# Kernel tuning notes

Measured on AMD Instinct MI355X. Metric: run time of the kernel, lower is better.

## Reference

```python
import jax, jax.numpy as jnp
import numpy as np

DIM = 1024        # model dim
HEADS = 1         # num_heads (fc1 in_features==1 forces this)
HDIM = DIM // HEADS
INNER = 16        # dim_inner
B, L = 2, 4096
ROPE_BASE = 32.0


def _apply_rope(x, pos, base):
    # x: [b, l, h, d]; standard rotate-half RoPE
    d = x.shape[-1]
    inv_freq = base ** (-jnp.arange(0, d, 2, dtype=jnp.float32) / d)   # [d/2]
    ang = pos[:, None].astype(jnp.float32) * inv_freq                  # [l, d/2]
    emb = jnp.concatenate([ang, ang], axis=-1)                         # [l, d]
    cos = jnp.cos(emb)[None, :, None, :].astype(x.dtype)
    sin = jnp.sin(emb)[None, :, None, :].astype(x.dtype)
    x1, x2 = x[..., : d // 2], x[..., d // 2:]
    rot = jnp.concatenate([-x2, x1], axis=-1)
    return x * cos + rot * sin


def setup_inputs() -> dict:
    key = jax.random.key(0)
    ks = jax.random.split(key, 7)
    hidden_states = jax.random.normal(ks[0], (B, L, DIM), dtype=jnp.float32)
    Wq = jax.random.normal(ks[1], (DIM, DIM), dtype=jnp.float32) * 0.02
    Wk = jax.random.normal(ks[2], (DIM, DIM), dtype=jnp.float32) * 0.02
    fc1_w = jax.random.normal(ks[3], (INNER, 1), dtype=jnp.float32) * 0.1
    fc1_b = jax.random.normal(ks[4], (INNER,), dtype=jnp.float32) * 0.1
    fc2_w = jax.random.normal(ks[5], (DIM, INNER), dtype=jnp.float32) * 0.1
    fc2_b = jax.random.normal(ks[6], (DIM,), dtype=jnp.float32) * 0.1
    return {"hidden_states": hidden_states, "Wq": Wq, "Wk": Wk,
            "fc1_w": fc1_w, "fc1_b": fc1_b, "fc2_w": fc2_w, "fc2_b": fc2_b}


def reference(hidden_states, Wq, Wk, fc1_w, fc1_b, fc2_w, fc2_b):
    b, l, _ = hidden_states.shape
    # projections, cast to bf16 as in the torch module
    q = (hidden_states @ Wq.T).reshape(b, l, HEADS, HDIM).astype(jnp.bfloat16)
    k = (hidden_states @ Wk.T).reshape(b, l, HEADS, HDIM).astype(jnp.bfloat16)
    pos = jnp.arange(l)
    q = _apply_rope(q, pos, ROPE_BASE)
    k = _apply_rope(k, pos, ROPE_BASE)
    # causal exp(QK) with NO softmax normalization; accumulate in fp32
    scores = jnp.einsum('bqhd,bkhd->bhqk',
                        q.astype(jnp.float32), k.astype(jnp.float32)) / (HDIM ** 0.5)
    causal = jnp.tril(jnp.ones((l, l), dtype=bool))                    # [l, l]
    exp_qk = jnp.where(causal[None, None], jnp.exp(scores), 0.0)       # [b, h, l, l]
    o = jnp.swapaxes(exp_qk.sum(axis=-1), 1, 2)                        # [b, l, h]
    # small MLP: h(=1) -> INNER -> DIM
    o = jax.nn.relu(o @ fc1_w.T + fc1_b)
    return o @ fc2_w.T + fc2_b                                         # [b, l, DIM]
```

## Files before the change

kernel.cpp:

```cpp
#include <hip/hip_runtime.h>
#include <hip/hip_bf16.h>

typedef __bf16 bf16_t;
typedef __bf16 bf16x4 __attribute__((ext_vector_type(4)));
typedef __bf16 bf16x8 __attribute__((ext_vector_type(8)));
typedef float f32x4 __attribute__((ext_vector_type(4)));

#define B_   2
#define L_   4096
#define DIM_ 1024
#define M_   (B_ * L_)
#define NTASK2_ 272

__device__ __forceinline__ void ld_g2l_16(const bf16_t* g, bf16_t* l) {
  __builtin_amdgcn_global_load_lds(
      (__attribute__((address_space(1))) void*)g,
      (__attribute__((address_space(3))) void*)l, 16, 0, 0);
}

__global__ void cvt_all(const float* __restrict__ hs, const float* __restrict__ wq,
                        const float* __restrict__ wk, bf16_t* __restrict__ hs_b,
                        bf16_t* __restrict__ wq_b, bf16_t* __restrict__ wk_b,
                        float* __restrict__ o) {
  const int N_HS = M_ * DIM_ / 4, N_W = DIM_ * DIM_ / 4;
  int i = blockIdx.x * blockDim.x + threadIdx.x;
  if (i < M_ / 4) ((float4*)o)[i] = float4{0.f, 0.f, 0.f, 0.f};
  const float* s; bf16_t* d; int idx;
  if (i < N_HS)            { s = hs; d = hs_b; idx = i; }
  else if (i < N_HS + N_W) { s = wq; d = wq_b; idx = i - N_HS; }
  else                     { s = wk; d = wk_b; idx = i - N_HS - N_W; }
  float4 v = ((const float4*)s)[idx];
  bf16x4 ov = { (bf16_t)v.x, (bf16_t)v.y, (bf16_t)v.z, (bf16_t)v.w };
  ((bf16x4*)d)[idx] = ov;
}

template <int BSEGS>
__device__ __forceinline__ void core256(const bf16_t* __restrict__ A,
                                        const bf16_t* __restrict__ B0,
                                        const bf16_t* __restrict__ B1,
                                        bf16_t* sm, bool active,
                                        f32x4 (&acc)[4][BSEGS / 2]) {
  constexpr int SEGS = 16 + BSEGS;
  constexpr int BUF  = SEGS * 512;
  const int tid  = threadIdx.x;
  const int wave = tid >> 6, lane = tid & 63;
  const int wm = wave >> 1, wn = wave & 1;
  const int quad = lane >> 4, l16 = lane & 15;
  const int srow = lane >> 2;
  const int scol = (((lane & 3) ^ ((lane >> 3) & 3)) * 8);
  const int rsw  = ((l16 >> 1) & 3) * 8;
  const int loff = l16 * 32 + ((quad * 8) ^ rsw);

  const bf16_t* gA0 = A + (size_t)(wave * 16 + srow) * DIM_ + scol;
  const bf16_t* gA1 = A + (size_t)((wave + 8) * 16 + srow) * DIM_ + scol;
  const bf16_t* gB0 = B0 + (size_t)(wave * 16 + srow) * DIM_ + scol;
  const bf16_t* gB1 = gB0;
  if constexpr (BSEGS == 16) gB1 = B1 + (size_t)(wave * 16 + srow) * DIM_ + scol;

  bf16_t* p0 = sm;
  bf16_t* p1 = sm + BUF;
  bf16_t* p2 = sm + 2 * BUF;

  auto stage = [&](int kk, bf16_t* buf) {
    ld_g2l_16(gA0 + kk, buf + wave * 512);
    ld_g2l_16(gA1 + kk, buf + (wave + 8) * 512);
    ld_g2l_16(gB0 + kk, buf + (16 + wave) * 512);
    if constexpr (BSEGS == 16) ld_g2l_16(gB1 + kk, buf + (24 + wave) * 512);
  };

  stage(0, p0);
  stage(32, p1);
  if constexpr (BSEGS == 16) asm volatile("s_waitcnt vmcnt(4)" ::: "memory");
  else                       asm volatile("s_waitcnt vmcnt(3)" ::: "memory");
  __builtin_amdgcn_s_barrier();

  for (int s = 0; s < 32; ++s) {
    bf16x8 aF[4], bF[BSEGS / 2];
    if (active) {
#pragma unroll
      for (int rf = 0; rf < 4; ++rf)
        aF[rf] = *(const bf16x8*)(p0 + (wm * 4 + rf) * 512 + loff);
#pragma unroll
      for (int cf = 0; cf < BSEGS / 2; ++cf) {
        int k = (cf & 3) + wn * 4 + (cf >> 2) * 8;
        bF[cf] = *(const bf16x8*)(p0 + (16 + k) * 512 + loff);
      }
    }
    if (s < 30) stage((s + 2) * 32, p2);
    __builtin_amdgcn_s_barrier();
    asm volatile("s_waitcnt lgkmcnt(0)" ::: "memory");
    __builtin_amdgcn_sched_barrier(0);
    if (active) {
      __builtin_amdgcn_s_setprio(1);
#pragma unroll
      for (int rf = 0; rf < 4; ++rf)
#pragma unroll
        for (int cf = 0; cf < BSEGS / 2; ++cf)
          acc[rf][cf] = __builtin_amdgcn_mfma_f32_16x16x32_bf16(
              aF[rf], bF[cf], acc[rf][cf], 0, 0, 0);
      __builtin_amdgcn_s_setprio(0);
    }
    if (s < 30) {
      if constexpr (BSEGS == 16) asm volatile("s_waitcnt vmcnt(4)" ::: "memory");
      else                       asm volatile("s_waitcnt vmcnt(3)" ::: "memory");
    } else if (s == 30) {
      asm volatile("s_waitcnt vmcnt(0)" ::: "memory");
    }
    __builtin_amdgcn_s_barrier();
    bf16_t* t0 = p0; p0 = p1; p1 = p2; p2 = t0;
  }
}

__global__ __launch_bounds__(512, 2)
void proj_gemm(const bf16_t* __restrict__ A, const bf16_t* __restrict__ Wqb,
               const bf16_t* __restrict__ Wkb, bf16_t* __restrict__ Cq,
               bf16_t* __restrict__ Ck) {
  __shared__ __attribute__((aligned(16))) bf16_t sm[3 * 32 * 512];
  const int bid = blockIdx.x;
  const int xcd = bid & 7, slot = bid >> 3;
  const int m0 = (xcd * 4 + (slot >> 3)) * 256;
  const int zn = slot & 7;
  const int z = zn >> 2, n0 = (zn & 3) * 128;
  const bf16_t* Wb = z ? Wkb : Wqb;
  bf16_t* Cm = z ? Ck : Cq;

  f32x4 acc[4][8] = {};
  core256<16>(A + (size_t)m0 * DIM_, Wb + (size_t)n0 * DIM_,
              Wb + (size_t)(n0 + 512) * DIM_, sm, true, acc);

  const int tid = threadIdx.x, wave = tid >> 6, lane = tid & 63;
  const int wm = wave >> 1, wn = wave & 1;
  const int quad = lane >> 4, l16 = lane & 15;

  float inv[4];
#pragma unroll
  for (int cf = 0; cf < 4; ++cf) {
    int j = n0 + wn * 64 + cf * 16 + l16;
    inv[cf] = exp2f((float)j * (-5.0f / 512.0f));
  }
#pragma unroll
  for (int rf = 0; rf < 4; ++rf)
#pragma unroll
    for (int r = 0; r < 4; ++r) {
      int m = m0 + wm * 64 + rf * 16 + quad * 4 + r;
      float posf = (float)(m & (L_ - 1));
#pragma unroll
      for (int cf = 0; cf < 4; ++cf) {
        int j = n0 + wn * 64 + cf * 16 + l16;
        float ang = posf * inv[cf];
        float c = cosf(ang), s = sinf(ang);
        float cb = (float)(bf16_t)c, sb = (float)(bf16_t)s;
        float x1 = (float)(bf16_t)acc[rf][cf][r];
        float x2 = (float)(bf16_t)acc[rf][cf + 4][r];
        Cm[(size_t)m * DIM_ + j]       = (bf16_t)(x1 * cb - x2 * sb);
        Cm[(size_t)m * DIM_ + j + 512] = (bf16_t)(x2 * cb + x1 * sb);
      }
    }
}

__global__ __launch_bounds__(512, 4)
void attn_rowsum(const bf16_t* __restrict__ Q, const bf16_t* __restrict__ Kc,
                 float* __restrict__ o) {
  __shared__ __attribute__((aligned(16))) bf16_t sm[3 * 24 * 512];
  int logical = (blockIdx.x & 7) * 68 + (blockIdx.x >> 3);
  int b = logical / NTASK2_;
  int t = logical - b * NTASK2_;
  int mi = (int)((sqrtf(4.0f * (float)t + 1.0f) - 1.0f) * 0.5f);
  while ((mi + 1) * (mi + 2) <= t) ++mi;
  while (mi * (mi + 1) > t) --mi;
  int nt = t - mi * (mi + 1);

  const int tid = threadIdx.x, wave = tid >> 6, lane = tid & 63;
  const int wm = wave >> 1, wn = wave & 1;
  const int quad = lane >> 4, l16 = lane & 15;

  const bf16_t* A  = Q  + (size_t)b * L_ * DIM_ + (size_t)mi * 256 * DIM_;
  const bf16_t* Bp = Kc + (size_t)b * L_ * DIM_ + (size_t)nt * 128 * DIM_;

  bool active = (mi * 256 + wm * 64 + 63) >= nt * 128;

  f32x4 acc[4][4] = {};
  core256<8>(A, Bp, nullptr, sm, active, acc);

  if (active) {
    const bool masked = (nt >= 2 * mi);
#pragma unroll
    for (int rf = 0; rf < 4; ++rf) {
#pragma unroll
      for (int r = 0; r < 4; ++r) {
        int grow = mi * 256 + wm * 64 + rf * 16 + quad * 4 + r;
        float sum = 0.0f;
#pragma unroll
        for (int cf = 0; cf < 4; ++cf) {
          int gcol = nt * 128 + wn * 64 + cf * 16 + l16;
          float e = __expf(acc[rf][cf][r] * 0.03125f);
          if (!masked || gcol <= grow) sum += e;
        }
        sum += __shfl_xor(sum, 1);
        sum += __shfl_xor(sum, 2);
        sum += __shfl_xor(sum, 4);
        sum += __shfl_xor(sum, 8);
        if (l16 == 0)
          atomicAdd(&o[b * L_ + grow], sum);
      }
    }
  }
}

__global__ __launch_bounds__(256)
void mlp_out_kernel(const float* __restrict__ o, const float* __restrict__ fc1_w,
                    const float* __restrict__ fc1_b, const float* __restrict__ fc2_w,
                    const float* __restrict__ fc2_b, float* __restrict__ out) {
  const int R = 16;
  int row0 = blockIdx.x * R;
  int tid = threadIdx.x;
  __shared__ float h[R][16];
  {
    int rl = tid >> 4, i = tid & 15;
    float s = o[row0 + rl];
    h[rl][i] = fmaxf(fc1_w[i] * s + fc1_b[i], 0.0f);
  }
  __syncthreads();
  int d = tid * 4;
  float w[4][16];
#pragma unroll
  for (int c = 0; c < 4; ++c)
#pragma unroll
    for (int i = 0; i < 16; ++i) w[c][i] = fc2_w[(d + c) * 16 + i];
  float4 bb = *(const float4*)(fc2_b + d);
  for (int rl = 0; rl < R; ++rl) {
    float4 v = bb;
#pragma unroll
    for (int i = 0; i < 16; ++i) {
      float hv = h[rl][i];
      v.x += w[0][i] * hv; v.y += w[1][i] * hv;
      v.z += w[2][i] * hv; v.w += w[3][i] * hv;
    }
    *(float4*)(out + (size_t)(row0 + rl) * DIM_ + d) = v;
  }
}

extern "C" void kernel_launch(void* const* d_in, const int* in_sizes, int n_in,
                              void* d_out, int out_size, void* d_ws, size_t ws_size,
                              hipStream_t stream) {
  const float* hs    = (const float*)d_in[0];
  const float* Wq    = (const float*)d_in[1];
  const float* Wk    = (const float*)d_in[2];
  const float* fc1_w = (const float*)d_in[3];
  const float* fc1_b = (const float*)d_in[4];
  const float* fc2_w = (const float*)d_in[5];
  const float* fc2_b = (const float*)d_in[6];
  float* out = (float*)d_out;

  char* ws = (char*)d_ws;
  bf16_t* hs_bf = (bf16_t*)ws; ws += (size_t)M_ * DIM_ * 2;
  bf16_t* wq_bf = (bf16_t*)ws; ws += (size_t)DIM_ * DIM_ * 2;
  bf16_t* wk_bf = (bf16_t*)ws; ws += (size_t)DIM_ * DIM_ * 2;
  bf16_t* q_bf  = (bf16_t*)ws; ws += (size_t)M_ * DIM_ * 2;
  bf16_t* k_bf  = (bf16_t*)ws; ws += (size_t)M_ * DIM_ * 2;
  float*  o     = (float*)ws;

  const int n4 = (M_ * DIM_ + 2 * DIM_ * DIM_) / 4;
  cvt_all<<<n4 / 256, 256, 0, stream>>>(hs, Wq, Wk, hs_bf, wq_bf, wk_bf, o);

  proj_gemm<<<256, 512, 0, stream>>>(hs_bf, wq_bf, wk_bf, q_bf, k_bf);

  attn_rowsum<<<544, 512, 0, stream>>>(q_bf, k_bf, o);

  mlp_out_kernel<<<M_ / 16, 256, 0, stream>>>(o, fc1_w, fc1_b, fc2_w, fc2_b, out);
}
```

Before: 257.1 us.

## Shrink projection GEMM tile to 256x128 and double grid for occupancy

The projection GEMM now computes 256x128 output tiles (64 columns plus their RoPE partner 64 columns 512 apart) instead of 256x256. That halves the per-block LDS and accumulator footprint, allows 4 blocks per CU, and launches 512 blocks instead of 256. The shared core routine is generalized so the attention kernel reuses it with a split B pointer. The trade-off is more A-tile reloads per output, since each A tile is now read by twice as many blocks.

```diff
diff --git a/kernel.cpp b/kernel.cpp
--- a/kernel.cpp
+++ b/kernel.cpp
@@ -34,14 +34,13 @@
   ((bf16x4*)d)[idx] = ov;
 }
 
-template <int BSEGS>
+template <bool PAIRK>
 __device__ __forceinline__ void core256(const bf16_t* __restrict__ A,
                                         const bf16_t* __restrict__ B0,
                                         const bf16_t* __restrict__ B1,
                                         bf16_t* sm, bool active,
-                                        f32x4 (&acc)[4][BSEGS / 2]) {
-  constexpr int SEGS = 16 + BSEGS;
-  constexpr int BUF  = SEGS * 512;
+                                        f32x4 (&acc)[4][4]) {
+  constexpr int BUF = 24 * 512;
   const int tid  = threadIdx.x;
   const int wave = tid >> 6, lane = tid & 63;
   const int wm = wave >> 1, wn = wave & 1;
@@ -53,9 +52,9 @@
 
   const bf16_t* gA0 = A + (size_t)(wave * 16 + srow) * DIM_ + scol;
   const bf16_t* gA1 = A + (size_t)((wave + 8) * 16 + srow) * DIM_ + scol;
-  const bf16_t* gB0 = B0 + (size_t)(wave * 16 + srow) * DIM_ + scol;
-  const bf16_t* gB1 = gB0;
-  if constexpr (BSEGS == 16) gB1 = B1 + (size_t)(wave * 16 + srow) * DIM_ + scol;
+  const bf16_t* gB  = (wave < 4)
+      ? B0 + (size_t)(wave * 16 + srow) * DIM_ + scol
+      : B1 + (size_t)((wave - 4) * 16 + srow) * DIM_ + scol;
 
   bf16_t* p0 = sm;
   bf16_t* p1 = sm + BUF;
@@ -64,25 +63,24 @@
   auto stage = [&](int kk, bf16_t* buf) {
     ld_g2l_16(gA0 + kk, buf + wave * 512);
     ld_g2l_16(gA1 + kk, buf + (wave + 8) * 512);
-    ld_g2l_16(gB0 + kk, buf + (16 + wave) * 512);
-    if constexpr (BSEGS == 16) ld_g2l_16(gB1 + kk, buf + (24 + wave) * 512);
+    ld_g2l_16(gB + kk, buf + (16 + wave) * 512);
   };
 
   stage(0, p0);
   stage(32, p1);
-  if constexpr (BSEGS == 16) asm volatile("s_waitcnt vmcnt(4)" ::: "memory");
-  else                       asm volatile("s_waitcnt vmcnt(3)" ::: "memory");
+  asm volatile("s_waitcnt vmcnt(3)" ::: "memory");
   __builtin_amdgcn_s_barrier();
 
   for (int s = 0; s < 32; ++s) {
-    bf16x8 aF[4], bF[BSEGS / 2];
+    bf16x8 aF[4], bF[4];
     if (active) {
 #pragma unroll
       for (int rf = 0; rf < 4; ++rf)
         aF[rf] = *(const bf16x8*)(p0 + (wm * 4 + rf) * 512 + loff);
 #pragma unroll
-      for (int cf = 0; cf < BSEGS / 2; ++cf) {
-        int k = (cf & 3) + wn * 4 + (cf >> 2) * 8;
+      for (int cf = 0; cf < 4; ++cf) {
+        int k = PAIRK ? ((cf & 1) + wn * 2 + (cf >> 1) * 4)
+                      : ((cf & 3) + wn * 4);
         bF[cf] = *(const bf16x8*)(p0 + (16 + k) * 512 + loff);
       }
     }
@@ -95,48 +93,44 @@
 #pragma unroll
       for (int rf = 0; rf < 4; ++rf)
 #pragma unroll
-        for (int cf = 0; cf < BSEGS / 2; ++cf)
+        for (int cf = 0; cf < 4; ++cf)
           acc[rf][cf] = __builtin_amdgcn_mfma_f32_16x16x32_bf16(
               aF[rf], bF[cf], acc[rf][cf], 0, 0, 0);
       __builtin_amdgcn_s_setprio(0);
     }
-    if (s < 30) {
-      if constexpr (BSEGS == 16) asm volatile("s_waitcnt vmcnt(4)" ::: "memory");
-      else                       asm volatile("s_waitcnt vmcnt(3)" ::: "memory");
-    } else if (s == 30) {
-      asm volatile("s_waitcnt vmcnt(0)" ::: "memory");
-    }
+    if (s < 30)       asm volatile("s_waitcnt vmcnt(3)" ::: "memory");
+    else if (s == 30) asm volatile("s_waitcnt vmcnt(0)" ::: "memory");
     __builtin_amdgcn_s_barrier();
     bf16_t* t0 = p0; p0 = p1; p1 = p2; p2 = t0;
   }
 }
 
-__global__ __launch_bounds__(512, 2)
+__global__ __launch_bounds__(512, 4)
 void proj_gemm(const bf16_t* __restrict__ A, const bf16_t* __restrict__ Wqb,
                const bf16_t* __restrict__ Wkb, bf16_t* __restrict__ Cq,
                bf16_t* __restrict__ Ck) {
-  __shared__ __attribute__((aligned(16))) bf16_t sm[3 * 32 * 512];
+  __shared__ __attribute__((aligned(16))) bf16_t sm[3 * 24 * 512];
   const int bid = blockIdx.x;
   const int xcd = bid & 7, slot = bid >> 3;
-  const int m0 = (xcd * 4 + (slot >> 3)) * 256;
-  const int zn = slot & 7;
-  const int z = zn >> 2, n0 = (zn & 3) * 128;
+  const int m0 = (xcd * 4 + (slot >> 4)) * 256;
+  const int zn = slot & 15;
+  const int z = zn >> 3, n0 = (zn & 7) * 64;
   const bf16_t* Wb = z ? Wkb : Wqb;
   bf16_t* Cm = z ? Ck : Cq;
 
-  f32x4 acc[4][8] = {};
-  core256<16>(A + (size_t)m0 * DIM_, Wb + (size_t)n0 * DIM_,
-              Wb + (size_t)(n0 + 512) * DIM_, sm, true, acc);
+  f32x4 acc[4][4] = {};
+  core256<true>(A + (size_t)m0 * DIM_, Wb + (size_t)n0 * DIM_,
+                Wb + (size_t)(n0 + 512) * DIM_, sm, true, acc);
 
   const int tid = threadIdx.x, wave = tid >> 6, lane = tid & 63;
   const int wm = wave >> 1, wn = wave & 1;
   const int quad = lane >> 4, l16 = lane & 15;
 
-  float inv[4];
-#pragma unroll
-  for (int cf = 0; cf < 4; ++cf) {
-    int j = n0 + wn * 64 + cf * 16 + l16;
-    inv[cf] = exp2f((float)j * (-5.0f / 512.0f));
+  float inv[2];
+#pragma unroll
+  for (int c2 = 0; c2 < 2; ++c2) {
+    int j = n0 + (c2 + wn * 2) * 16 + l16;
+    inv[c2] = exp2f((float)j * (-5.0f / 512.0f));
   }
 #pragma unroll
   for (int rf = 0; rf < 4; ++rf)
@@ -145,13 +139,13 @@
       int m = m0 + wm * 64 + rf * 16 + quad * 4 + r;
       float posf = (float)(m & (L_ - 1));
 #pragma unroll
-      for (int cf = 0; cf < 4; ++cf) {
-        int j = n0 + wn * 64 + cf * 16 + l16;
-        float ang = posf * inv[cf];
+      for (int c2 = 0; c2 < 2; ++c2) {
+        int j = n0 + (c2 + wn * 2) * 16 + l16;
+        float ang = posf * inv[c2];
         float c = cosf(ang), s = sinf(ang);
         float cb = (float)(bf16_t)c, sb = (float)(bf16_t)s;
-        float x1 = (float)(bf16_t)acc[rf][cf][r];
-        float x2 = (float)(bf16_t)acc[rf][cf + 4][r];
+        float x1 = (float)(bf16_t)acc[rf][c2][r];
+        float x2 = (float)(bf16_t)acc[rf][c2 + 2][r];
         Cm[(size_t)m * DIM_ + j]       = (bf16_t)(x1 * cb - x2 * sb);
         Cm[(size_t)m * DIM_ + j + 512] = (bf16_t)(x2 * cb + x1 * sb);
       }
@@ -180,7 +174,7 @@
   bool active = (mi * 256 + wm * 64 + 63) >= nt * 128;
 
   f32x4 acc[4][4] = {};
-  core256<8>(A, Bp, nullptr, sm, active, acc);
+  core256<false>(A, Bp, Bp + (size_t)64 * DIM_, sm, active, acc);
 
   if (active) {
     const bool masked = (nt >= 2 * mi);
@@ -263,7 +257,7 @@
   const int n4 = (M_ * DIM_ + 2 * DIM_ * DIM_) / 4;
   cvt_all<<<n4 / 256, 256, 0, stream>>>(hs, Wq, Wk, hs_bf, wq_bf, wk_bf, o);
 
-  proj_gemm<<<256, 512, 0, stream>>>(hs_bf, wq_bf, wk_bf, q_bf, k_bf);
+  proj_gemm<<<512, 512, 0, stream>>>(hs_bf, wq_bf, wk_bf, q_bf, k_bf);
 
   attn_rowsum<<<544, 512, 0, stream>>>(q_bf, k_bf, o);
 
```

Result: faster. 236.2 us (-8.1%).
